# Optimization experiments

Measured on AMD Instinct MI355X. Metric: run time of the kernel, lower is better.

The kernel has to match this reference:

```python
import jax, jax.numpy as jnp
import numpy as np

EMBED = 256
HEADS = 8
N, L, S = 4, 128, 64


def setup_inputs() -> dict:
    key = jax.random.key(0)
    ks = jax.random.split(key, 9)
    values = jax.random.normal(ks[0], (N, L, S, EMBED), dtype=jnp.float32)
    keys_ = jax.random.normal(ks[1], (N, L, S, EMBED), dtype=jnp.float32)
    query = jax.random.normal(ks[2], (N, L, S, EMBED), dtype=jnp.float32)
    mask = jax.random.randint(ks[3], (N, 1, L, L, 1), 0, 2, dtype=jnp.int32)
    sc = 1.0 / np.sqrt(EMBED)
    Wq = jax.random.normal(ks[4], (EMBED, EMBED), dtype=jnp.float32) * sc
    Wk = jax.random.normal(ks[5], (EMBED, EMBED), dtype=jnp.float32) * sc
    Wv = jax.random.normal(ks[6], (EMBED, EMBED), dtype=jnp.float32) * sc
    Wo = jax.random.normal(ks[7], (HEADS * EMBED, EMBED), dtype=jnp.float32) * (1.0 / np.sqrt(HEADS * EMBED))
    bo = jnp.zeros((EMBED,), dtype=jnp.float32)
    return {"values": values, "keys": keys_, "query": query, "mask": mask,
            "Wq": Wq, "Wk": Wk, "Wv": Wv, "Wo": Wo, "bo": bo}


def reference(values, keys, query, mask, Wq, Wk, Wv, Wo, bo):
    n, q_len, s_len, d = query.shape
    k_len = keys.shape[1]
    h = HEADS
    # Per-head projections share one weight (expand happens BEFORE Linear in
    # the original), so compute each projection once and broadcast over heads.
    q = jnp.einsum('nqsd,de->nqse', query, Wq)   # [N,Q,S,D]
    k = jnp.einsum('nksd,de->nkse', keys, Wk)    # [N,K,S,D]
    v = jnp.einsum('nksd,de->nkse', values, Wv)  # [N,K,S,D]
    # energy: nqshd,nkshd->nhqks ; identical across h pre-mask
    energy = jnp.einsum('nqsd,nksd->nqks', q, k)            # [N,Q,K,S]
    energy = jnp.broadcast_to(energy[:, None], (n, h, q_len, k_len, s_len))
    energy = jnp.where(mask == 0, jnp.float32(-1e20), energy)
    attn = jax.nn.softmax(energy / jnp.sqrt(jnp.float32(d)), axis=3)  # over K
    # out: nhqls,nlshd->nqshd
    out = jnp.einsum('nhqks,nksd->nqshd', attn, v)
    out = out.reshape(n, q_len, s_len, h * d)
    return out @ Wo + bo
```

## Files before the change

### kernel.cpp

```cpp
#include <hip/hip_runtime.h>
#include <hip/hip_bf16.h>


using bf16x4 = __attribute__((ext_vector_type(4))) __bf16;
using bf16x8 = __attribute__((ext_vector_type(8))) __bf16;
using f32x4  = __attribute__((ext_vector_type(4))) float;

#define MFMA(a, b, c) __builtin_amdgcn_mfma_f32_16x16x32_bf16((a), (b), (c), 0, 0, 0)

__device__ __forceinline__ bf16x8 cvt8(float4 f0, float4 f1) {
  bf16x8 a;
  a[0]=(__bf16)f0.x; a[1]=(__bf16)f0.y; a[2]=(__bf16)f0.z; a[3]=(__bf16)f0.w;
  a[4]=(__bf16)f1.x; a[5]=(__bf16)f1.y; a[6]=(__bf16)f1.z; a[7]=(__bf16)f1.w;
  return a;
}

__global__ __launch_bounds__(512) void prep_mm(
    const float* __restrict__ Wq, const float* __restrict__ Wk,
    const float* __restrict__ Wv, const float* __restrict__ Wo,
    __bf16* __restrict__ mqk, __bf16* __restrict__ mvo) {
  __shared__ float wt[256 * 17];
  const int t = threadIdx.x, lane = t & 63, w = t >> 6;
  const int lr = lane & 15, g = lane >> 4;
  const int ct = blockIdx.x;
  const bool isV = blockIdx.y != 0;
  const float* Aw = isV ? Wv : Wq;
  __bf16* dst = isV ? mvo : mqk;

  bf16x8 af0[8], af1[8];
#pragma unroll
  for (int k8 = 0; k8 < 8; ++k8) {
    const float* p0 = Aw + (size_t)((2 * w)     * 16 + lr) * 256 + k8 * 32 + g * 8;
    const float* p1 = Aw + (size_t)((2 * w + 1) * 16 + lr) * 256 + k8 * 32 + g * 8;
    af0[k8] = cvt8(*(const float4*)p0, *(const float4*)(p0 + 4));
    af1[k8] = cvt8(*(const float4*)p1, *(const float4*)(p1 + 4));
  }
  bf16x8 bf[8];
  if (!isV) {
#pragma unroll
    for (int k8 = 0; k8 < 8; ++k8) {
      const float* p = Wk + (size_t)(ct * 16 + lr) * 256 + k8 * 32 + g * 8;
      bf[k8] = cvt8(*(const float4*)p, *(const float4*)(p + 4));
    }
  } else {
#pragma unroll
    for (int i = 0; i < 8; ++i) {
      int cell = i * 512 + t, e2 = cell >> 4, eol = cell & 15;
      float ssum = 0.f;
#pragma unroll
      for (int h = 0; h < 8; ++h)
        ssum += Wo[((size_t)(h * 256 + e2)) * 256 + ct * 16 + eol];
      wt[e2 * 17 + eol] = ssum;
    }
    __syncthreads();
#pragma unroll
    for (int k8 = 0; k8 < 8; ++k8)
#pragma unroll
      for (int jj = 0; jj < 8; ++jj)
        bf[k8][jj] = (__bf16)wt[(k8 * 32 + g * 8 + jj) * 17 + lr];
  }
  f32x4 a0 = {0.f,0.f,0.f,0.f}, a1 = {0.f,0.f,0.f,0.f};
#pragma unroll
  for (int k8 = 0; k8 < 8; ++k8) {
    a0 = MFMA(af0[k8], bf[k8], a0);
    a1 = MFMA(af1[k8], bf[k8], a1);
  }
#pragma unroll
  for (int rtl = 0; rtl < 2; ++rtl) {
    const f32x4& ac = rtl ? a1 : a0;
    bf16x4 pb;
#pragma unroll
    for (int j = 0; j < 4; ++j) pb[j] = (__bf16)ac[j];
    size_t off = (size_t)ct * 4096 + w * 512 +
                 ((2 * rtl + (g >> 1)) * 16 + lr) * 8 + 4 * (g & 1);
    *reinterpret_cast<bf16x4*>(dst + off) = pb;
  }
}

__global__ __launch_bounds__(1024, 4) void fused_attn(
    const float* __restrict__ Xv, const float* __restrict__ Xk,
    const float* __restrict__ Xq, const int* __restrict__ mask,
    const __bf16* __restrict__ mqk, const __bf16* __restrict__ mvo,
    const float* __restrict__ bo, float* __restrict__ out) {
  extern __shared__ char lds[];
  char*  A   = lds;
  char*  B   = lds + 65536;
  float* scr = reinterpret_cast<float*>(lds + 131072);
  const int t = threadIdx.x, lane = t & 63, w = t >> 6;
  const int lr = lane & 15, g = lane >> 4;
  const int sl = blockIdx.x, n = sl >> 6, s = sl & 63;
  const int qt = w & 7, kh = w >> 3;

  auto fill = [&](const float* __restrict__ X, float4* vr) {
#pragma unroll
    for (int i = 0; i < 4; ++i) {
      int f8 = i * 1024 + t, row = f8 >> 5, c8 = f8 & 31;
      const float* src = X + ((size_t)(n * 8192 + row * 64 + s)) * 256 + c8 * 8;
      vr[2 * i]     = *reinterpret_cast<const float4*>(src);
      vr[2 * i + 1] = *reinterpret_cast<const float4*>(src + 4);
    }
  };
  auto flushv = [&](const float4* vr) {
#pragma unroll
    for (int i = 0; i < 4; ++i) {
      int f8 = i * 1024 + t, row = f8 >> 5, c8 = f8 & 31;
      bf16x8 b;
      b[0]=(__bf16)vr[2*i].x;   b[1]=(__bf16)vr[2*i].y;
      b[2]=(__bf16)vr[2*i].z;   b[3]=(__bf16)vr[2*i].w;
      b[4]=(__bf16)vr[2*i+1].x; b[5]=(__bf16)vr[2*i+1].y;
      b[6]=(__bf16)vr[2*i+1].z; b[7]=(__bf16)vr[2*i+1].w;
      *reinterpret_cast<bf16x8*>(
          A + row * 512 + ((c8 * 16) ^ ((row & 7) << 4))) = b;
    }
  };

  bf16x8 wf[8];
  {
    const bf16x8* wp = reinterpret_cast<const bf16x8*>(mqk);
#pragma unroll
    for (int k8 = 0; k8 < 8; ++k8) wf[k8] = wp[(w * 8 + k8) * 64 + lane];
  }
  {
    float4 vr[8];
    fill(Xq, vr);
    flushv(vr);
  }
  __syncthreads();

  float4 vrp[8];
  fill(Xk, vrp);
#pragma unroll
  for (int ct = 0; ct < 8; ++ct) {
    bf16x8 xf[8];
#pragma unroll
    for (int k8 = 0; k8 < 8; ++k8) {
      int brow = ct * 16 + lr;
      xf[k8] = *reinterpret_cast<const bf16x8*>(
          A + brow * 512 + ((k8 * 64 + g * 16) ^ ((brow & 7) << 4)));
    }
    f32x4 a = {0.f,0.f,0.f,0.f};
#pragma unroll
    for (int k8 = 0; k8 < 8; ++k8) a = MFMA(wf[k8], xf[k8], a);
    bf16x4 pb;
#pragma unroll
    for (int j = 0; j < 4; ++j) pb[j] = (__bf16)a[j];
    *reinterpret_cast<bf16x4*>(
        B + ct * 8192 + (w >> 1) * 1024 +
        (lr + 16 * (2 * (w & 1) + (g >> 1))) * 16 + (g & 1) * 8) = pb;
  }
  __syncthreads();

  bf16x8 af[8];
#pragma unroll
  for (int k8 = 0; k8 < 8; ++k8)
    af[k8] = *reinterpret_cast<const bf16x8*>(B + qt * 8192 + k8 * 1024 + lane * 16);
  flushv(vrp);
  __syncthreads();

  fill(Xv, vrp);
  int mreg[4][4];
#pragma unroll
  for (int ct = 0; ct < 4; ++ct)
#pragma unroll
    for (int j = 0; j < 4; ++j)
      mreg[ct][j] = mask[((size_t)n * 128 + qt * 16 + 4 * g + j) * 128 +
                         (kh * 4 + ct) * 16 + lr];
  f32x4 sacc[4];
#pragma unroll
  for (int ct = 0; ct < 4; ++ct) {
    int brow = (kh * 4 + ct) * 16 + lr;
    bf16x8 xf[8];
#pragma unroll
    for (int k8 = 0; k8 < 8; ++k8)
      xf[k8] = *reinterpret_cast<const bf16x8*>(
          A + brow * 512 + ((k8 * 64 + g * 16) ^ ((brow & 7) << 4)));
    f32x4 a = {0.f,0.f,0.f,0.f};
#pragma unroll
    for (int k8 = 0; k8 < 8; ++k8) a = MFMA(af[k8], xf[k8], a);
    sacc[ct] = a;
  }

  float p[4][4], mxv[4], smv[4];
#pragma unroll
  for (int j = 0; j < 4; ++j) {
    float mx = -3e38f;
#pragma unroll
    for (int ct = 0; ct < 4; ++ct) {
      float sv = mreg[ct][j] ? sacc[ct][j] * 0.0625f : -6.25e18f;
      p[ct][j] = sv;
      mx = fmaxf(mx, sv);
    }
#pragma unroll
    for (int o = 1; o < 16; o <<= 1) mx = fmaxf(mx, __shfl_xor(mx, o));
    float sum = 0.f;
#pragma unroll
    for (int ct = 0; ct < 4; ++ct) {
      float e = __expf(p[ct][j] - mx);
      p[ct][j] = e;
      sum += e;
    }
#pragma unroll
    for (int o = 1; o < 16; o <<= 1) sum += __shfl_xor(sum, o);
    mxv[j] = mx; smv[j] = sum;
  }
  if (lr == 0) {
#pragma unroll
    for (int j = 0; j < 4; ++j) {
      scr[w * 32 + g * 8 + j * 2]     = mxv[j];
      scr[w * 32 + g * 8 + j * 2 + 1] = smv[j];
    }
  }
  __syncthreads();

  {
    int pw = w ^ 8;
#pragma unroll
    for (int j = 0; j < 4; ++j) {
      float pmx = scr[pw * 32 + g * 8 + j * 2];
      float psm = scr[pw * 32 + g * 8 + j * 2 + 1];
      float M = fmaxf(mxv[j], pmx);
      float tot = smv[j] * __expf(mxv[j] - M) + psm * __expf(pmx - M);
      float scale = __expf(mxv[j] - M) / tot;
#pragma unroll
      for (int ct = 0; ct < 4; ++ct) p[ct][j] *= scale;
    }
  }
#pragma unroll
  for (int ct = 0; ct < 4; ++ct) {
    int cg = kh * 4 + ct;
    char* bse = B + qt * 4096 + (cg >> 1) * 1024 +
                (16 * ((cg * 2 + (lr >> 3)) & 3)) * 16 + (lr & 7) * 2;
#pragma unroll
    for (int j = 0; j < 4; ++j)
      *reinterpret_cast<__bf16*>(bse + (4 * g + j) * 16) = (__bf16)p[ct][j];
  }
  flushv(vrp);
  __syncthreads();

  bf16x8 vf[8];
  {
    const bf16x8* wp = reinterpret_cast<const bf16x8*>(mvo);
#pragma unroll
    for (int k8 = 0; k8 < 8; ++k8) vf[k8] = wp[(w * 8 + k8) * 64 + lane];
  }
  bf16x8 pa[4];
#pragma unroll
  for (int kk8 = 0; kk8 < 4; ++kk8)
    pa[kk8] = *reinterpret_cast<const bf16x8*>(B + qt * 4096 + kk8 * 1024 + lane * 16);
  __syncthreads();

  float br[8];
#pragma unroll
  for (int e8 = 0; e8 < 8; ++e8) br[e8] = bo[(kh * 8 + e8) * 16 + lr];
#pragma unroll
  for (int ct = 0; ct < 8; ++ct) {
    int brow = ct * 16 + lr;
    bf16x8 xf[8];
#pragma unroll
    for (int k8 = 0; k8 < 8; ++k8)
      xf[k8] = *reinterpret_cast<const bf16x8*>(
          A + brow * 512 + ((k8 * 64 + g * 16) ^ ((brow & 7) << 4)));
    f32x4 a = {0.f,0.f,0.f,0.f};
#pragma unroll
    for (int k8 = 0; k8 < 8; ++k8) a = MFMA(vf[k8], xf[k8], a);
    char* bse = B + w * 4096 + (ct >> 1) * 1024 +
                (16 * ((ct * 2 + (lr >> 3)) & 3)) * 16 + (lr & 7) * 2;
#pragma unroll
    for (int j = 0; j < 4; ++j)
      *reinterpret_cast<__bf16*>(bse + (4 * g + j) * 16) = (__bf16)a[j];
  }
  __syncthreads();

#pragma unroll
  for (int e8 = 0; e8 < 8; ++e8) {
    int et = kh * 8 + e8;
    bf16x8 bfr[4];
#pragma unroll
    for (int kk8 = 0; kk8 < 4; ++kk8)
      bfr[kk8] = *reinterpret_cast<const bf16x8*>(
          B + et * 4096 + kk8 * 1024 + lane * 16);
    f32x4 a = {0.f,0.f,0.f,0.f};
#pragma unroll
    for (int kk8 = 0; kk8 < 4; ++kk8) a = MFMA(pa[kk8], bfr[kk8], a);
#pragma unroll
    for (int j = 0; j < 4; ++j) {
      int q = qt * 16 + 4 * g + j;
      out[((size_t)n * 8192 + q * 64 + s) * 256 + et * 16 + lr] = a[j] + br[e8];
    }
  }
}

extern "C" void kernel_launch(void* const* d_in, const int* in_sizes, int n_in,
                              void* d_out, int out_size, void* d_ws, size_t ws_size,
                              hipStream_t stream) {
  const float* values = (const float*)d_in[0];
  const float* keys   = (const float*)d_in[1];
  const float* query  = (const float*)d_in[2];
  const int*   mask   = (const int*)d_in[3];
  const float* Wq     = (const float*)d_in[4];
  const float* Wk     = (const float*)d_in[5];
  const float* Wv     = (const float*)d_in[6];
  const float* Wo     = (const float*)d_in[7];
  const float* bo     = (const float*)d_in[8];
  float* out = (float*)d_out;

  char* w = (char*)d_ws;
  __bf16* mqk = (__bf16*)w; w += 131072;
  __bf16* mvo = (__bf16*)w; w += 131072;

  prep_mm<<<dim3(16, 2), 512, 0, stream>>>(Wq, Wk, Wv, Wo, mqk, mvo);
  fused_attn<<<256, 1024, 133120, stream>>>(values, keys, query, mask,
                                            mqk, mvo, bo, out);
}
```

Measured before the change: 55.59 us.

## Switch to 32x32x16 MFMA tiles with 512-thread blocks and vectorized I/O

Both kernels now use 32x32x16 bf16 MFMA instead of 16x16x32. The attention block shrinks from 1024 to 512 threads, and each wave owns 32-row tiles. The LDS staging images, the mask loads (int4) and the output stores (float4 with bias) are relaid to match. Softmax row reductions now need only a single cross-half shuffle. In exchange, the kernel holds more registers per wave and needs larger dynamic LDS (160 KB), which limits how many blocks can share a CU.

```diff
diff --git a/kernel.cpp b/kernel.cpp
--- a/kernel.cpp
+++ b/kernel.cpp
@@ -4,9 +4,9 @@
 
 using bf16x4 = __attribute__((ext_vector_type(4))) __bf16;
 using bf16x8 = __attribute__((ext_vector_type(8))) __bf16;
-using f32x4  = __attribute__((ext_vector_type(4))) float;
-
-#define MFMA(a, b, c) __builtin_amdgcn_mfma_f32_16x16x32_bf16((a), (b), (c), 0, 0, 0)
+using f32x16 = __attribute__((ext_vector_type(16))) float;
+
+#define MFMA32(a, b, c) __builtin_amdgcn_mfma_f32_32x32x16_bf16((a), (b), (c), 0, 0, 0)
 
 __device__ __forceinline__ bf16x8 cvt8(float4 f0, float4 f1) {
   bf16x8 a;
@@ -14,87 +14,89 @@
   a[4]=(__bf16)f1.x; a[5]=(__bf16)f1.y; a[6]=(__bf16)f1.z; a[7]=(__bf16)f1.w;
   return a;
 }
-
-__global__ __launch_bounds__(512) void prep_mm(
+__device__ __forceinline__ f32x16 zero16() {
+  f32x16 z;
+#pragma unroll
+  for (int j = 0; j < 16; ++j) z[j] = 0.f;
+  return z;
+}
+
+__global__ __launch_bounds__(512) void prep_pack(
     const float* __restrict__ Wq, const float* __restrict__ Wk,
     const float* __restrict__ Wv, const float* __restrict__ Wo,
     __bf16* __restrict__ mqk, __bf16* __restrict__ mvo) {
-  __shared__ float wt[256 * 17];
+  __shared__ float wt[256 * 33];
   const int t = threadIdx.x, lane = t & 63, w = t >> 6;
-  const int lr = lane & 15, g = lane >> 4;
+  const int lq = lane & 31, hl = lane >> 5;
   const int ct = blockIdx.x;
   const bool isV = blockIdx.y != 0;
+  if (isV) {
+#pragma unroll
+    for (int i = 0; i < 16; ++i) {
+      int cell = i * 512 + t;
+      int e2 = cell >> 5, eol = cell & 31;
+      float ssum = 0.f;
+#pragma unroll
+      for (int h = 0; h < 8; ++h)
+        ssum += Wo[((size_t)(h * 256 + e2)) * 256 + ct * 32 + eol];
+      wt[e2 * 33 + eol] = ssum;
+    }
+    __syncthreads();
+  }
   const float* Aw = isV ? Wv : Wq;
-  __bf16* dst = isV ? mvo : mqk;
-
-  bf16x8 af0[8], af1[8];
-#pragma unroll
-  for (int k8 = 0; k8 < 8; ++k8) {
-    const float* p0 = Aw + (size_t)((2 * w)     * 16 + lr) * 256 + k8 * 32 + g * 8;
-    const float* p1 = Aw + (size_t)((2 * w + 1) * 16 + lr) * 256 + k8 * 32 + g * 8;
-    af0[k8] = cvt8(*(const float4*)p0, *(const float4*)(p0 + 4));
-    af1[k8] = cvt8(*(const float4*)p1, *(const float4*)(p1 + 4));
-  }
-  bf16x8 bf[8];
+  bf16x8 afr[16], bfr[16];
+#pragma unroll
+  for (int ks = 0; ks < 16; ++ks) {
+    const float* p = Aw + (size_t)(w * 32 + lq) * 256 + ks * 16 + hl * 8;
+    afr[ks] = cvt8(*(const float4*)p, *(const float4*)(p + 4));
+  }
   if (!isV) {
 #pragma unroll
-    for (int k8 = 0; k8 < 8; ++k8) {
-      const float* p = Wk + (size_t)(ct * 16 + lr) * 256 + k8 * 32 + g * 8;
-      bf[k8] = cvt8(*(const float4*)p, *(const float4*)(p + 4));
+    for (int ks = 0; ks < 16; ++ks) {
+      const float* p = Wk + (size_t)(ct * 32 + lq) * 256 + ks * 16 + hl * 8;
+      bfr[ks] = cvt8(*(const float4*)p, *(const float4*)(p + 4));
     }
   } else {
 #pragma unroll
-    for (int i = 0; i < 8; ++i) {
-      int cell = i * 512 + t, e2 = cell >> 4, eol = cell & 15;
-      float ssum = 0.f;
-#pragma unroll
-      for (int h = 0; h < 8; ++h)
-        ssum += Wo[((size_t)(h * 256 + e2)) * 256 + ct * 16 + eol];
-      wt[e2 * 17 + eol] = ssum;
-    }
-    __syncthreads();
-#pragma unroll
-    for (int k8 = 0; k8 < 8; ++k8)
+    for (int ks = 0; ks < 16; ++ks)
 #pragma unroll
       for (int jj = 0; jj < 8; ++jj)
-        bf[k8][jj] = (__bf16)wt[(k8 * 32 + g * 8 + jj) * 17 + lr];
-  }
-  f32x4 a0 = {0.f,0.f,0.f,0.f}, a1 = {0.f,0.f,0.f,0.f};
-#pragma unroll
-  for (int k8 = 0; k8 < 8; ++k8) {
-    a0 = MFMA(af0[k8], bf[k8], a0);
-    a1 = MFMA(af1[k8], bf[k8], a1);
-  }
-#pragma unroll
-  for (int rtl = 0; rtl < 2; ++rtl) {
-    const f32x4& ac = rtl ? a1 : a0;
-    bf16x4 pb;
-#pragma unroll
-    for (int j = 0; j < 4; ++j) pb[j] = (__bf16)ac[j];
-    size_t off = (size_t)ct * 4096 + w * 512 +
-                 ((2 * rtl + (g >> 1)) * 16 + lr) * 8 + 4 * (g & 1);
-    *reinterpret_cast<bf16x4*>(dst + off) = pb;
-  }
-}
-
-__global__ __launch_bounds__(1024, 4) void fused_attn(
+        bfr[ks][jj] = (__bf16)wt[(ks * 16 + hl * 8 + jj) * 33 + lq];
+  }
+  f32x16 acc = zero16();
+#pragma unroll
+  for (int ks = 0; ks < 16; ++ks) acc = MFMA32(afr[ks], bfr[ks], acc);
+  char* dstb = (char*)(isV ? mvo : mqk);
+#pragma unroll
+  for (int a = 0; a < 4; ++a) {
+    bf16x4 v;
+#pragma unroll
+    for (int j = 0; j < 4; ++j) v[j] = (__bf16)acc[4 * a + j];
+    *(bf16x4*)(dstb + ct * 16384 + (2 * w + (a >> 1)) * 1024 +
+               (lq + 32 * (a & 1)) * 16 + hl * 8) = v;
+  }
+}
+
+__global__ __launch_bounds__(512) void fused_attn(
     const float* __restrict__ Xv, const float* __restrict__ Xk,
     const float* __restrict__ Xq, const int* __restrict__ mask,
     const __bf16* __restrict__ mqk, const __bf16* __restrict__ mvo,
     const float* __restrict__ bo, float* __restrict__ out) {
   extern __shared__ char lds[];
-  char*  A   = lds;
-  char*  B   = lds + 65536;
-  float* scr = reinterpret_cast<float*>(lds + 131072);
+  char* A     = lds;
+  char* Timg  = lds + 65536;
+  char* Pimg  = lds + 65536;
+  char* B1img = lds + 98304;
+  float* scr  = (float*)(lds + 98304);
   const int t = threadIdx.x, lane = t & 63, w = t >> 6;
-  const int lr = lane & 15, g = lane >> 4;
+  const int lq = lane & 31, hl = lane >> 5;
+  const int qt = w & 3, kh = w >> 2;
   const int sl = blockIdx.x, n = sl >> 6, s = sl & 63;
-  const int qt = w & 7, kh = w >> 3;
 
   auto fill = [&](const float* __restrict__ X, float4* vr) {
 #pragma unroll
-    for (int i = 0; i < 4; ++i) {
-      int f8 = i * 1024 + t, row = f8 >> 5, c8 = f8 & 31;
+    for (int i = 0; i < 8; ++i) {
+      int f8 = i * 512 + t, row = f8 >> 5, c8 = f8 & 31;
       const float* src = X + ((size_t)(n * 8192 + row * 64 + s)) * 256 + c8 * 8;
       vr[2 * i]     = *reinterpret_cast<const float4*>(src);
       vr[2 * i + 1] = *reinterpret_cast<const float4*>(src + 4);
@@ -102,190 +104,170 @@
   };
   auto flushv = [&](const float4* vr) {
 #pragma unroll
-    for (int i = 0; i < 4; ++i) {
-      int f8 = i * 1024 + t, row = f8 >> 5, c8 = f8 & 31;
+    for (int i = 0; i < 8; ++i) {
+      int f8 = i * 512 + t, row = f8 >> 5, c8 = f8 & 31;
       bf16x8 b;
       b[0]=(__bf16)vr[2*i].x;   b[1]=(__bf16)vr[2*i].y;
       b[2]=(__bf16)vr[2*i].z;   b[3]=(__bf16)vr[2*i].w;
       b[4]=(__bf16)vr[2*i+1].x; b[5]=(__bf16)vr[2*i+1].y;
       b[6]=(__bf16)vr[2*i+1].z; b[7]=(__bf16)vr[2*i+1].w;
-      *reinterpret_cast<bf16x8*>(
-          A + row * 512 + ((c8 * 16) ^ ((row & 7) << 4))) = b;
+      *reinterpret_cast<bf16x8*>(A + row * 512 + ((c8 * 16) ^ ((row & 7) << 4))) = b;
     }
   };
-
-  bf16x8 wf[8];
+  auto xfrag = [&](int brow, int ks) -> bf16x8 {
+    return *reinterpret_cast<const bf16x8*>(
+        A + brow * 512 + ((ks * 32 + hl * 16) ^ ((brow & 7) << 4)));
+  };
+
+  { float4 vr[16]; fill(Xq, vr); flushv(vr); }
+  __syncthreads();
+
+  float4 vrp[16];
+  fill(Xk, vrp);
   {
     const bf16x8* wp = reinterpret_cast<const bf16x8*>(mqk);
-#pragma unroll
-    for (int k8 = 0; k8 < 8; ++k8) wf[k8] = wp[(w * 8 + k8) * 64 + lane];
-  }
+    bf16x8 wf[16];
+#pragma unroll
+    for (int ks = 0; ks < 16; ++ks) wf[ks] = wp[(w * 16 + ks) * 64 + lane];
+#pragma unroll
+    for (int rt = 0; rt < 4; ++rt) {
+      f32x16 acc = zero16();
+#pragma unroll
+      for (int ks = 0; ks < 16; ++ks)
+        acc = MFMA32(wf[ks], xfrag(rt * 32 + lq, ks), acc);
+#pragma unroll
+      for (int a = 0; a < 4; ++a) {
+        bf16x4 v;
+#pragma unroll
+        for (int j = 0; j < 4; ++j) v[j] = (__bf16)acc[4 * a + j];
+        *(bf16x4*)(Timg + rt * 16384 + (2 * w + (a >> 1)) * 1024 +
+                   (lq + 32 * (a & 1)) * 16 + hl * 8) = v;
+      }
+    }
+  }
+  __syncthreads();
+
+  bf16x8 af[16];
+#pragma unroll
+  for (int ks = 0; ks < 16; ++ks)
+    af[ks] = *reinterpret_cast<const bf16x8*>(Timg + qt * 16384 + ks * 1024 + lane * 16);
+  flushv(vrp);
+  __syncthreads();
+
+  fill(Xv, vrp);
+  int ms[2][16];
+#pragma unroll
+  for (int c = 0; c < 2; ++c)
+#pragma unroll
+    for (int a = 0; a < 4; ++a) {
+      int4 m = *reinterpret_cast<const int4*>(
+          mask + ((size_t)n * 128 + qt * 32 + lq) * 128 +
+          (2 * kh + c) * 32 + 8 * a + 4 * hl);
+      ms[c][4*a] = m.x; ms[c][4*a+1] = m.y; ms[c][4*a+2] = m.z; ms[c][4*a+3] = m.w;
+    }
+  f32x16 acc[2];
+#pragma unroll
+  for (int c = 0; c < 2; ++c) {
+    acc[c] = zero16();
+    int kt = 2 * kh + c;
+#pragma unroll
+    for (int ks = 0; ks < 16; ++ks)
+      acc[c] = MFMA32(xfrag(kt * 32 + lq, ks), af[ks], acc[c]);
+  }
+  float mx = -3e38f;
+#pragma unroll
+  for (int c = 0; c < 2; ++c)
+#pragma unroll
+    for (int r = 0; r < 16; ++r) {
+      float sv = ms[c][r] ? acc[c][r] * 0.0625f : -6.25e18f;
+      acc[c][r] = sv;
+      mx = fmaxf(mx, sv);
+    }
+  mx = fmaxf(mx, __shfl_xor(mx, 32));
+  float sum = 0.f;
+#pragma unroll
+  for (int c = 0; c < 2; ++c)
+#pragma unroll
+    for (int r = 0; r < 16; ++r) {
+      float e = __expf(acc[c][r] - mx);
+      acc[c][r] = e;
+      sum += e;
+    }
+  sum += __shfl_xor(sum, 32);
+  if (lane < 32) {
+    float2* s2 = reinterpret_cast<float2*>(scr);
+    s2[(qt * 2 + kh) * 32 + lane] = make_float2(mx, sum);
+  }
+  __syncthreads();
+
   {
-    float4 vr[8];
-    fill(Xq, vr);
-    flushv(vr);
-  }
-  __syncthreads();
-
-  float4 vrp[8];
-  fill(Xk, vrp);
-#pragma unroll
-  for (int ct = 0; ct < 8; ++ct) {
-    bf16x8 xf[8];
-#pragma unroll
-    for (int k8 = 0; k8 < 8; ++k8) {
-      int brow = ct * 16 + lr;
-      xf[k8] = *reinterpret_cast<const bf16x8*>(
-          A + brow * 512 + ((k8 * 64 + g * 16) ^ ((brow & 7) << 4)));
-    }
-    f32x4 a = {0.f,0.f,0.f,0.f};
-#pragma unroll
-    for (int k8 = 0; k8 < 8; ++k8) a = MFMA(wf[k8], xf[k8], a);
-    bf16x4 pb;
-#pragma unroll
-    for (int j = 0; j < 4; ++j) pb[j] = (__bf16)a[j];
-    *reinterpret_cast<bf16x4*>(
-        B + ct * 8192 + (w >> 1) * 1024 +
-        (lr + 16 * (2 * (w & 1) + (g >> 1))) * 16 + (g & 1) * 8) = pb;
-  }
-  __syncthreads();
-
-  bf16x8 af[8];
-#pragma unroll
-  for (int k8 = 0; k8 < 8; ++k8)
-    af[k8] = *reinterpret_cast<const bf16x8*>(B + qt * 8192 + k8 * 1024 + lane * 16);
+    float2 pr = reinterpret_cast<const float2*>(scr)[(qt * 2 + (kh ^ 1)) * 32 + lq];
+    float M = fmaxf(mx, pr.x);
+    float tot = sum * __expf(mx - M) + pr.y * __expf(pr.x - M);
+    float scale = __expf(mx - M) / tot;
+#pragma unroll
+    for (int c = 0; c < 2; ++c)
+#pragma unroll
+      for (int r = 0; r < 16; ++r) acc[c][r] *= scale;
+  }
+#pragma unroll
+  for (int c = 0; c < 2; ++c)
+#pragma unroll
+    for (int a = 0; a < 4; ++a) {
+      bf16x4 v;
+#pragma unroll
+      for (int j = 0; j < 4; ++j) v[j] = (__bf16)acc[c][4 * a + j];
+      *(bf16x4*)(Pimg + qt * 8192 + ((2 * kh + c) * 2 + (a >> 1)) * 1024 +
+                 (lq + 32 * (a & 1)) * 16 + hl * 8) = v;
+    }
   flushv(vrp);
-  __syncthreads();
-
-  fill(Xv, vrp);
-  int mreg[4][4];
-#pragma unroll
-  for (int ct = 0; ct < 4; ++ct)
-#pragma unroll
-    for (int j = 0; j < 4; ++j)
-      mreg[ct][j] = mask[((size_t)n * 128 + qt * 16 + 4 * g + j) * 128 +
-                         (kh * 4 + ct) * 16 + lr];
-  f32x4 sacc[4];
-#pragma unroll
-  for (int ct = 0; ct < 4; ++ct) {
-    int brow = (kh * 4 + ct) * 16 + lr;
-    bf16x8 xf[8];
-#pragma unroll
-    for (int k8 = 0; k8 < 8; ++k8)
-      xf[k8] = *reinterpret_cast<const bf16x8*>(
-          A + brow * 512 + ((k8 * 64 + g * 16) ^ ((brow & 7) << 4)));
-    f32x4 a = {0.f,0.f,0.f,0.f};
-#pragma unroll
-    for (int k8 = 0; k8 < 8; ++k8) a = MFMA(af[k8], xf[k8], a);
-    sacc[ct] = a;
-  }
-
-  float p[4][4], mxv[4], smv[4];
-#pragma unroll
-  for (int j = 0; j < 4; ++j) {
-    float mx = -3e38f;
-#pragma unroll
-    for (int ct = 0; ct < 4; ++ct) {
-      float sv = mreg[ct][j] ? sacc[ct][j] * 0.0625f : -6.25e18f;
-      p[ct][j] = sv;
-      mx = fmaxf(mx, sv);
-    }
-#pragma unroll
-    for (int o = 1; o < 16; o <<= 1) mx = fmaxf(mx, __shfl_xor(mx, o));
-    float sum = 0.f;
-#pragma unroll
-    for (int ct = 0; ct < 4; ++ct) {
-      float e = __expf(p[ct][j] - mx);
-      p[ct][j] = e;
-      sum += e;
-    }
-#pragma unroll
-    for (int o = 1; o < 16; o <<= 1) sum += __shfl_xor(sum, o);
-    mxv[j] = mx; smv[j] = sum;
-  }
-  if (lr == 0) {
-#pragma unroll
-    for (int j = 0; j < 4; ++j) {
-      scr[w * 32 + g * 8 + j * 2]     = mxv[j];
-      scr[w * 32 + g * 8 + j * 2 + 1] = smv[j];
-    }
-  }
-  __syncthreads();
-
+  bf16x8 vf[16];
   {
-    int pw = w ^ 8;
-#pragma unroll
-    for (int j = 0; j < 4; ++j) {
-      float pmx = scr[pw * 32 + g * 8 + j * 2];
-      float psm = scr[pw * 32 + g * 8 + j * 2 + 1];
-      float M = fmaxf(mxv[j], pmx);
-      float tot = smv[j] * __expf(mxv[j] - M) + psm * __expf(pmx - M);
-      float scale = __expf(mxv[j] - M) / tot;
-#pragma unroll
-      for (int ct = 0; ct < 4; ++ct) p[ct][j] *= scale;
-    }
-  }
-#pragma unroll
-  for (int ct = 0; ct < 4; ++ct) {
-    int cg = kh * 4 + ct;
-    char* bse = B + qt * 4096 + (cg >> 1) * 1024 +
-                (16 * ((cg * 2 + (lr >> 3)) & 3)) * 16 + (lr & 7) * 2;
-#pragma unroll
-    for (int j = 0; j < 4; ++j)
-      *reinterpret_cast<__bf16*>(bse + (4 * g + j) * 16) = (__bf16)p[ct][j];
-  }
-  flushv(vrp);
-  __syncthreads();
-
-  bf16x8 vf[8];
-  {
-    const bf16x8* wp = reinterpret_cast<const bf16x8*>(mvo);
-#pragma unroll
-    for (int k8 = 0; k8 < 8; ++k8) vf[k8] = wp[(w * 8 + k8) * 64 + lane];
-  }
-  bf16x8 pa[4];
-#pragma unroll
-  for (int kk8 = 0; kk8 < 4; ++kk8)
-    pa[kk8] = *reinterpret_cast<const bf16x8*>(B + qt * 4096 + kk8 * 1024 + lane * 16);
-  __syncthreads();
-
-  float br[8];
-#pragma unroll
-  for (int e8 = 0; e8 < 8; ++e8) br[e8] = bo[(kh * 8 + e8) * 16 + lr];
-#pragma unroll
-  for (int ct = 0; ct < 8; ++ct) {
-    int brow = ct * 16 + lr;
-    bf16x8 xf[8];
-#pragma unroll
-    for (int k8 = 0; k8 < 8; ++k8)
-      xf[k8] = *reinterpret_cast<const bf16x8*>(
-          A + brow * 512 + ((k8 * 64 + g * 16) ^ ((brow & 7) << 4)));
-    f32x4 a = {0.f,0.f,0.f,0.f};
-#pragma unroll
-    for (int k8 = 0; k8 < 8; ++k8) a = MFMA(vf[k8], xf[k8], a);
-    char* bse = B + w * 4096 + (ct >> 1) * 1024 +
-                (16 * ((ct * 2 + (lr >> 3)) & 3)) * 16 + (lr & 7) * 2;
-#pragma unroll
-    for (int j = 0; j < 4; ++j)
-      *reinterpret_cast<__bf16*>(bse + (4 * g + j) * 16) = (__bf16)a[j];
-  }
-  __syncthreads();
-
-#pragma unroll
-  for (int e8 = 0; e8 < 8; ++e8) {
-    int et = kh * 8 + e8;
-    bf16x8 bfr[4];
-#pragma unroll
-    for (int kk8 = 0; kk8 < 4; ++kk8)
-      bfr[kk8] = *reinterpret_cast<const bf16x8*>(
-          B + et * 4096 + kk8 * 1024 + lane * 16);
-    f32x4 a = {0.f,0.f,0.f,0.f};
-#pragma unroll
-    for (int kk8 = 0; kk8 < 4; ++kk8) a = MFMA(pa[kk8], bfr[kk8], a);
-#pragma unroll
-    for (int j = 0; j < 4; ++j) {
-      int q = qt * 16 + 4 * g + j;
-      out[((size_t)n * 8192 + q * 64 + s) * 256 + et * 16 + lr] = a[j] + br[e8];
+    const bf16x8* vp = reinterpret_cast<const bf16x8*>(mvo);
+#pragma unroll
+    for (int ks = 0; ks < 16; ++ks) vf[ks] = vp[(w * 16 + ks) * 64 + lane];
+  }
+  __syncthreads();
+
+#pragma unroll
+  for (int rt = 0; rt < 4; ++rt) {
+    f32x16 a1 = zero16();
+#pragma unroll
+    for (int ks = 0; ks < 16; ++ks)
+      a1 = MFMA32(xfrag(rt * 32 + lq, ks), vf[ks], a1);
+#pragma unroll
+    for (int a = 0; a < 4; ++a) {
+      bf16x4 v;
+#pragma unroll
+      for (int j = 0; j < 4; ++j) v[j] = (__bf16)a1[4 * a + j];
+      *(bf16x4*)(B1img + w * 8192 + (2 * rt + (a >> 1)) * 1024 +
+                 (lq + 32 * (a & 1)) * 16 + hl * 8) = v;
+    }
+  }
+  __syncthreads();
+
+  bf16x8 pa[8];
+#pragma unroll
+  for (int ks = 0; ks < 8; ++ks)
+    pa[ks] = *reinterpret_cast<const bf16x8*>(Pimg + qt * 8192 + ks * 1024 + lane * 16);
+  float* orow = out + ((size_t)(n * 8192) + (qt * 32 + lq) * 64 + s) * 256;
+#pragma unroll
+  for (int el = 0; el < 4; ++el) {
+    int et = kh * 4 + el;
+    f32x16 a2 = zero16();
+#pragma unroll
+    for (int ks = 0; ks < 8; ++ks) {
+      bf16x8 bfr = *reinterpret_cast<const bf16x8*>(
+          B1img + et * 8192 + ks * 1024 + lane * 16);
+      a2 = MFMA32(bfr, pa[ks], a2);
+    }
+#pragma unroll
+    for (int a = 0; a < 4; ++a) {
+      float4 bv = *reinterpret_cast<const float4*>(bo + et * 32 + 8 * a + 4 * hl);
+      float4 st;
+      st.x = a2[4*a]   + bv.x; st.y = a2[4*a+1] + bv.y;
+      st.z = a2[4*a+2] + bv.z; st.w = a2[4*a+3] + bv.w;
+      *reinterpret_cast<float4*>(orow + et * 32 + 8 * a + 4 * hl) = st;
     }
   }
 }
@@ -308,7 +290,7 @@
   __bf16* mqk = (__bf16*)w; w += 131072;
   __bf16* mvo = (__bf16*)w; w += 131072;
 
-  prep_mm<<<dim3(16, 2), 512, 0, stream>>>(Wq, Wk, Wv, Wo, mqk, mvo);
-  fused_attn<<<256, 1024, 133120, stream>>>(values, keys, query, mask,
-                                            mqk, mvo, bo, out);
-}
+  prep_pack<<<dim3(8, 2), 512, 0, stream>>>(Wq, Wk, Wv, Wo, mqk, mvo);
+  fused_attn<<<256, 512, 163840, stream>>>(values, keys, query, mask,
+                                           mqk, mvo, bo, out);
+}
```

After: 54.13 us. 2.6% less time.
